# Kernel optimization log

Measured on AMD Instinct MI355X. Metric: run time of the kernel, lower is better.

Reference implementation:

```python
import jax, jax.numpy as jnp
import numpy as np

N_NODES = 50000
N_EDGES = 800000
IN_DIM, HID_DIM, OUT_DIM = 128, 128, 256


def _gcn_conv(x, W, b, src, dst, num_nodes):
    # PyG GCNConv: h = D^{-1/2} (A + I) D^{-1/2} X W + b (self-loops already in src/dst)
    h = x @ W  # (N, F_out)
    ones = jnp.ones(src.shape[0], dtype=h.dtype)
    deg = jax.ops.segment_sum(ones, dst, num_segments=num_nodes)
    dinv = jnp.where(deg > 0, jax.lax.rsqrt(deg), 0.0)
    norm = dinv[src] * dinv[dst]  # (E,)
    msg = h[src] * norm[:, None]  # (E, F_out) gather
    out = jax.ops.segment_sum(msg, dst, num_segments=num_nodes)  # scatter-add
    return out + b


def setup_inputs() -> dict:
    key = jax.random.key(0)
    ks = jax.random.split(key, 6)
    x = jax.random.normal(ks[0], (N_NODES, IN_DIM), dtype=jnp.float32)
    edge_index = jax.random.randint(ks[1], (2, N_EDGES), 0, N_NODES, dtype=jnp.int64)
    W1 = jax.random.normal(ks[2], (IN_DIM, HID_DIM), dtype=jnp.float32) / np.sqrt(IN_DIM)
    b1 = jnp.zeros((HID_DIM,), jnp.float32)
    W2 = jax.random.normal(ks[3], (HID_DIM, OUT_DIM), dtype=jnp.float32) / np.sqrt(HID_DIM)
    b2 = jnp.zeros((OUT_DIM,), jnp.float32)
    Wa = jax.random.normal(ks[4], (OUT_DIM, 1), dtype=jnp.float32) / np.sqrt(OUT_DIM)
    ba = jnp.zeros((1,), jnp.float32)
    return {"x": x, "edge_index": edge_index, "W1": W1, "b1": b1, "W2": W2, "b2": b2, "Wa": Wa, "ba": ba}


def reference(x, edge_index, W1, b1, W2, b2, Wa, ba):
    n = x.shape[0]
    loops = jnp.arange(n, dtype=edge_index.dtype)
    src = jnp.concatenate([edge_index[0], loops])
    dst = jnp.concatenate([edge_index[1], loops])
    h = jax.nn.relu(_gcn_conv(x, W1, b1, src, dst, n))
    # dropout is a no-op in eval mode
    node_embeddings = jax.nn.relu(_gcn_conv(h, W2, b2, src, dst, n))
    logits = node_embeddings @ Wa + ba  # (N, 1)
    attn = jax.nn.softmax(logits, axis=0)  # softmax over nodes
    graph_embedding = jnp.sum(node_embeddings * attn, axis=0, keepdims=True)  # (1, OUT_DIM)
    return (node_embeddings, graph_embedding)
```

## Files before the change

kernel.cpp:

```cpp
#include <hip/hip_runtime.h>
#include <hip/hip_fp16.h>
#include <math.h>

typedef __attribute__((ext_vector_type(8))) short bf16x8;
typedef __attribute__((ext_vector_type(4))) float f32x4;

static __device__ __forceinline__ unsigned short f2bf(float x) {
    unsigned u = __float_as_uint(x);
    unsigned r = (u + 0x7FFF + ((u >> 16) & 1)) >> 16;
    return (unsigned short)r;
}
static __device__ __forceinline__ float bf2f(unsigned short h) {
    return __uint_as_float(((unsigned)h) << 16);
}
static __device__ __forceinline__ void addh8(float a[8], uint4 v) {
    float2 f;
    f = __half22float2(*(const __half2*)&v.x); a[0] += f.x; a[1] += f.y;
    f = __half22float2(*(const __half2*)&v.y); a[2] += f.x; a[3] += f.y;
    f = __half22float2(*(const __half2*)&v.z); a[4] += f.x; a[5] += f.y;
    f = __half22float2(*(const __half2*)&v.w); a[6] += f.x; a[7] += f.y;
}


__global__ __launch_bounds__(256) void count_deg_kernel(const int* __restrict__ dst, int E,
                                                        int* __restrict__ deg,
                                                        int* __restrict__ epos) {
    int e = blockIdx.x * 256 + threadIdx.x;
    if (e < E) epos[e] = atomicAdd(&deg[dst[e]], 1);
}

__global__ __launch_bounds__(256) void scan_partial_kernel(const int* __restrict__ deg, int n,
                                                           int* __restrict__ partials) {
    int idx = blockIdx.x * 1024 + threadIdx.x * 4;
    int4 v = make_int4(0, 0, 0, 0);
    if (idx + 3 < n) v = *(const int4*)(deg + idx);
    else {
        if (idx < n) v.x = deg[idx];
        if (idx + 1 < n) v.y = deg[idx + 1];
        if (idx + 2 < n) v.z = deg[idx + 2];
    }
    int s = v.x + v.y + v.z + v.w;
    for (int off = 1; off < 64; off <<= 1) s += __shfl_xor(s, off);
    __shared__ int sm[4];
    int wave = threadIdx.x >> 6;
    if ((threadIdx.x & 63) == 0) sm[wave] = s;
    __syncthreads();
    if (threadIdx.x == 0) partials[blockIdx.x] = sm[0] + sm[1] + sm[2] + sm[3];
}

__global__ __launch_bounds__(64) void scan_offsets_kernel(const int* __restrict__ partials, int nb,
                                                          int* __restrict__ poff,
                                                          int* __restrict__ rowptr, int n) {
    int t = threadIdx.x;
    int v = (t < nb) ? partials[t] : 0;
    int s = v;
    for (int off = 1; off < 64; off <<= 1) {
        int u = __shfl_up(s, off);
        if (t >= off) s += u;
    }
    poff[t] = s - v;
    if (t == 63) rowptr[n] = s;
}

__global__ __launch_bounds__(256) void scan_final_kernel(const int* __restrict__ deg, int n,
                                                         const int* __restrict__ poff,
                                                         int* __restrict__ rowptr) {
    int idx = blockIdx.x * 1024 + threadIdx.x * 4;
    int4 v = make_int4(0, 0, 0, 0);
    if (idx + 3 < n) v = *(const int4*)(deg + idx);
    else {
        if (idx < n) v.x = deg[idx];
        if (idx + 1 < n) v.y = deg[idx + 1];
        if (idx + 2 < n) v.z = deg[idx + 2];
    }
    int tsum = v.x + v.y + v.z + v.w;
    int lane = threadIdx.x & 63, wave = threadIdx.x >> 6;
    int s = tsum;
    for (int off = 1; off < 64; off <<= 1) {
        int u = __shfl_up(s, off);
        if (lane >= off) s += u;
    }
    __shared__ int wsum[4];
    if (lane == 63) wsum[wave] = s;
    __syncthreads();
    int base = poff[blockIdx.x];
    for (int w = 0; w < wave; ++w) base += wsum[w];
    int e0 = base + s - tsum;
    int4 o;
    o.x = e0; o.y = e0 + v.x; o.z = o.y + v.y; o.w = o.z + v.z;
    if (idx + 3 < n) *(int4*)(rowptr + idx) = o;
    else {
        if (idx < n) rowptr[idx] = o.x;
        if (idx + 1 < n) rowptr[idx + 1] = o.y;
        if (idx + 2 < n) rowptr[idx + 2] = o.z;
    }
}

__global__ __launch_bounds__(256) void scatter_kernel(const int* __restrict__ src,
                                                      const int* __restrict__ dst,
                                                      const int* __restrict__ epos, int E,
                                                      const int* __restrict__ rowptr,
                                                      int* __restrict__ csrsrc) {
    int e = blockIdx.x * 256 + threadIdx.x;
    if (e < E) csrsrc[rowptr[dst[e]] + epos[e]] = src[e];
}


__global__ __launch_bounds__(256) void dinv_prescale_kernel(const float* __restrict__ x,
                                                            const int* __restrict__ deg,
                                                            float* __restrict__ dinv,
                                                            __half2* __restrict__ xs16, int n) {
    int node = blockIdx.x * 4 + (threadIdx.x >> 6);
    int lane = threadIdx.x & 63;
    if (node >= n) return;
    float di = rsqrtf((float)(deg[node] + 1));
    if (lane == 0) dinv[node] = di;
    float2 v = *(const float2*)(x + (size_t)node * 128 + (lane << 1));
    xs16[(size_t)node * 64 + lane] = __floats2half2_rn(di * v.x, di * v.y);
}


__global__ __launch_bounds__(256) void wconvert_kernel(const float* __restrict__ W1,
                                                       const float* __restrict__ W2,
                                                       unsigned short* __restrict__ w1h,
                                                       unsigned short* __restrict__ w1l,
                                                       unsigned short* __restrict__ w2h,
                                                       unsigned short* __restrict__ w2l) {
    int i = blockIdx.x * 256 + threadIdx.x;
    if (i < 128 * 128) {
        int nn = i >> 7, k = i & 127;
        float v = W1[k * 128 + nn];
        unsigned short h = f2bf(v);
        w1h[i] = h;
        w1l[i] = f2bf(v - bf2f(h));
    } else if (i < 128 * 128 + 256 * 128) {
        int j = i - 128 * 128;
        int nn = j >> 7, k = j & 127;
        float v = W2[k * 256 + nn];
        unsigned short h = f2bf(v);
        w2h[j] = h;
        w2l[j] = f2bf(v - bf2f(h));
    }
}


__global__ __launch_bounds__(256) void aggregate_kernel(const unsigned short* __restrict__ X16,
                                                        const float* __restrict__ dinv,
                                                        const int* __restrict__ rowptr,
                                                        const int* __restrict__ deg,
                                                        const int* __restrict__ csrsrc,
                                                        unsigned short* __restrict__ outH,
                                                        unsigned short* __restrict__ outL, int n) {
    int node = blockIdx.x * 16 + (threadIdx.x >> 4);
    int sl = threadIdx.x & 15;
    if (node >= n) return;
    const uint4* Xv = (const uint4*)X16;
    float acc[8] = {0.f, 0.f, 0.f, 0.f, 0.f, 0.f, 0.f, 0.f};
    addh8(acc, Xv[(size_t)node * 16 + sl]);
    int e0 = rowptr[node];
    int e1 = e0 + deg[node];
    int e = e0;
    for (; e + 4 <= e1; e += 4) {
        int s0 = csrsrc[e], s1 = csrsrc[e + 1], s2 = csrsrc[e + 2], s3 = csrsrc[e + 3];
        uint4 v0 = Xv[(size_t)s0 * 16 + sl];
        uint4 v1 = Xv[(size_t)s1 * 16 + sl];
        uint4 v2 = Xv[(size_t)s2 * 16 + sl];
        uint4 v3 = Xv[(size_t)s3 * 16 + sl];
        addh8(acc, v0); addh8(acc, v1); addh8(acc, v2); addh8(acc, v3);
    }
    for (; e < e1; ++e) {
        uint4 v = Xv[(size_t)csrsrc[e] * 16 + sl];
        addh8(acc, v);
    }
    float di = dinv[node];
    unsigned short h[8], l[8];
#pragma unroll
    for (int j = 0; j < 8; ++j) {
        float f = di * acc[j];
        h[j] = f2bf(f);
        l[j] = f2bf(f - bf2f(h[j]));
    }
    uint4 hv, lv;
    hv.x = (unsigned)h[0] | ((unsigned)h[1] << 16);
    hv.y = (unsigned)h[2] | ((unsigned)h[3] << 16);
    hv.z = (unsigned)h[4] | ((unsigned)h[5] << 16);
    hv.w = (unsigned)h[6] | ((unsigned)h[7] << 16);
    lv.x = (unsigned)l[0] | ((unsigned)l[1] << 16);
    lv.y = (unsigned)l[2] | ((unsigned)l[3] << 16);
    lv.z = (unsigned)l[4] | ((unsigned)l[5] << 16);
    lv.w = (unsigned)l[6] | ((unsigned)l[7] << 16);
    *(uint4*)(outH + (size_t)node * 128 + sl * 8) = hv;
    *(uint4*)(outL + (size_t)node * 128 + sl * 8) = lv;
}


template <int N, bool SCALE_DINV, bool DO_LOGITS, bool OUT_F16>
__global__ __launch_bounds__(256, 3) void gemm_mfma(const unsigned short* __restrict__ Ah,
                                                    const unsigned short* __restrict__ Al,
                                                    const unsigned short* __restrict__ Bth,
                                                    const unsigned short* __restrict__ Btl,
                                                    const float* __restrict__ bias,
                                                    void* __restrict__ Cout, int M,
                                                    const float* __restrict__ dinv,
                                                    const float* __restrict__ Wa,
                                                    float* __restrict__ logits) {
    const int t = threadIdx.x;
    const int lane = t & 63;
    const int wave = t >> 6;
    const int wrow = wave >> 1;
    const int wcol = wave & 1;
    const int lq = lane >> 4;
    const int lm = lane & 15;
    const int row0 = blockIdx.x * 128;
    const int col0 = blockIdx.y * 128;

    int ar[4];
#pragma unroll
    for (int rt = 0; rt < 4; ++rt) {
        int r = row0 + wrow * 64 + rt * 16 + lm;
        ar[rt] = (r < M) ? r : (M - 1);
    }
    const int cb = col0 + wcol * 64 + lm;

    f32x4 acc[4][4] = {};
    float lacc[4][4] = {};

#pragma unroll
    for (int kq = 0; kq < 4; ++kq) {
        const int ko = kq * 32 + lq * 8;
        bf16x8 a_h[4], a_l[4], b_h[4], b_l[4];
#pragma unroll
        for (int rt = 0; rt < 4; ++rt) {
            const size_t o = (size_t)ar[rt] * 128 + ko;
            a_h[rt] = *(const bf16x8*)(Ah + o);
            a_l[rt] = *(const bf16x8*)(Al + o);
        }
#pragma unroll
        for (int ct = 0; ct < 4; ++ct) {
            const size_t o = (size_t)(cb + ct * 16) * 128 + ko;
            b_h[ct] = *(const bf16x8*)(Bth + o);
            b_l[ct] = *(const bf16x8*)(Btl + o);
        }
#pragma unroll
        for (int rt = 0; rt < 4; ++rt)
#pragma unroll
            for (int ct = 0; ct < 4; ++ct) {
                acc[rt][ct] = __builtin_amdgcn_mfma_f32_16x16x32_bf16(a_h[rt], b_h[ct], acc[rt][ct], 0, 0, 0);
                acc[rt][ct] = __builtin_amdgcn_mfma_f32_16x16x32_bf16(a_l[rt], b_h[ct], acc[rt][ct], 0, 0, 0);
                acc[rt][ct] = __builtin_amdgcn_mfma_f32_16x16x32_bf16(a_h[rt], b_l[ct], acc[rt][ct], 0, 0, 0);
            }
    }

#pragma unroll
    for (int ct = 0; ct < 4; ++ct) {
        int col = col0 + wcol * 64 + ct * 16 + lm;
        float bc = bias[col];
        float wac = DO_LOGITS ? Wa[col] : 0.f;
#pragma unroll
        for (int rt = 0; rt < 4; ++rt) {
            int rowb = row0 + wrow * 64 + rt * 16 + lq * 4;
#pragma unroll
            for (int reg = 0; reg < 4; ++reg) {
                int gr = rowb + reg;
                if (gr < M) {
                    float o = fmaxf(acc[rt][ct][reg] + bc, 0.f);
                    if (SCALE_DINV) o *= dinv[gr];
                    if (OUT_F16) ((__half*)Cout)[(size_t)gr * N + col] = __float2half(o);
                    else ((float*)Cout)[(size_t)gr * N + col] = o;
                    if (DO_LOGITS) lacc[rt][reg] += o * wac;
                }
            }
        }
    }

    if (DO_LOGITS) {
#pragma unroll
        for (int rt = 0; rt < 4; ++rt)
#pragma unroll
            for (int reg = 0; reg < 4; ++reg) {
                float s = lacc[rt][reg];
                s += __shfl_xor(s, 1);
                s += __shfl_xor(s, 2);
                s += __shfl_xor(s, 4);
                s += __shfl_xor(s, 8);
                int gr = row0 + wrow * 64 + rt * 16 + lq * 4 + reg;
                if (lm == 0 && gr < M) atomicAdd(&logits[gr], s);
            }
    }
}


__global__ __launch_bounds__(256) void maxsum_kernel(const float* __restrict__ logits, int n,
                                                     float2* __restrict__ part) {
    float m = -INFINITY, s = 0.f;
    for (int i = blockIdx.x * 256 + threadIdx.x; i < n; i += gridDim.x * 256) {
        float v = logits[i];
        if (v > m) { s = s * expf(m - v) + 1.f; m = v; }
        else s += expf(v - m);
    }
    __shared__ float sm[256], ss[256];
    sm[threadIdx.x] = m; ss[threadIdx.x] = s;
    __syncthreads();
    for (int off = 128; off > 0; off >>= 1) {
        if (threadIdx.x < off) {
            float m1 = sm[threadIdx.x], s1 = ss[threadIdx.x];
            float m2 = sm[threadIdx.x + off], s2 = ss[threadIdx.x + off];
            float M = fmaxf(m1, m2);
            sm[threadIdx.x] = M;
            ss[threadIdx.x] = s1 * expf(m1 - M) + s2 * expf(m2 - M);
        }
        __syncthreads();
    }
    if (threadIdx.x == 0) part[blockIdx.x] = make_float2(sm[0], ss[0]);
}

__global__ __launch_bounds__(64) void merge_kernel(const float2* __restrict__ part,
                                                   float* __restrict__ gms) {
    __shared__ float sm[64], ss[64];
    float2 p = part[threadIdx.x];
    sm[threadIdx.x] = p.x; ss[threadIdx.x] = p.y;
    __syncthreads();
    for (int off = 32; off > 0; off >>= 1) {
        if (threadIdx.x < off) {
            float m1 = sm[threadIdx.x], s1 = ss[threadIdx.x];
            float m2 = sm[threadIdx.x + off], s2 = ss[threadIdx.x + off];
            float M = fmaxf(m1, m2);
            sm[threadIdx.x] = M;
            ss[threadIdx.x] = s1 * expf(m1 - M) + s2 * expf(m2 - M);
        }
        __syncthreads();
    }
    if (threadIdx.x == 0) { gms[0] = sm[0]; gms[1] = ss[0]; }
}

__global__ __launch_bounds__(256) void weighted_sum_kernel(const float* __restrict__ emb,
                                                           const float* __restrict__ logits,
                                                           const float* __restrict__ gms,
                                                           float* __restrict__ gpart, int n) {
    float g = gms[0];
    int wave = threadIdx.x >> 6;
    int lane = threadIdx.x & 63;
    int stride = gridDim.x * 4;
    float4 acc = make_float4(0.f, 0.f, 0.f, 0.f);
#pragma unroll 2
    for (int r = blockIdx.x * 4 + wave; r < n; r += stride) {
        float w = expf(logits[r] - g);
        float4 v = *(const float4*)(emb + (size_t)r * 256 + (lane << 2));
        acc.x += w * v.x; acc.y += w * v.y; acc.z += w * v.z; acc.w += w * v.w;
    }
    __shared__ float4 sm[256];
    sm[threadIdx.x] = acc;
    __syncthreads();
    if (wave == 0) {
        float4 a = sm[lane], b = sm[64 + lane], c = sm[128 + lane], d = sm[192 + lane];
        float4 s;
        s.x = (a.x + b.x) + (c.x + d.x);
        s.y = (a.y + b.y) + (c.y + d.y);
        s.z = (a.z + b.z) + (c.z + d.z);
        s.w = (a.w + b.w) + (c.w + d.w);
        *(float4*)(gpart + (size_t)blockIdx.x * 256 + (lane << 2)) = s;
    }
}

__global__ __launch_bounds__(256) void reduce_gpart_kernel(const float* __restrict__ gpart,
                                                           float* __restrict__ outTail, int nb) {
    int rows = nb / gridDim.x;
    int r0 = blockIdx.x * rows;
    float s = 0.f;
    for (int r = r0; r < r0 + rows; ++r) s += gpart[(size_t)r * 256 + threadIdx.x];
    atomicAdd(&outTail[threadIdx.x], s);
}

__global__ __launch_bounds__(256) void normalize_kernel(float* __restrict__ outTail,
                                                        const float* __restrict__ gms) {
    outTail[threadIdx.x] = outTail[threadIdx.x] / gms[1];
}


extern "C" void kernel_launch(void* const* d_in, const int* in_sizes, int n_in,
                              void* d_out, int out_size, void* d_ws, size_t ws_size,
                              hipStream_t stream) {
    const float* x  = (const float*)d_in[0];
    const int* ei   = (const int*)d_in[1];
    const float* W1 = (const float*)d_in[2];
    const float* b1 = (const float*)d_in[3];
    const float* W2 = (const float*)d_in[4];
    const float* b2 = (const float*)d_in[5];
    const float* Wa = (const float*)d_in[6];
    float* out = (float*)d_out;

    const int n = in_sizes[0] / 128;
    const int E = in_sizes[1] / 2;
    const int* srcA = ei;
    const int* dstA = ei + E;
    const int nb = (n + 1023) / 1024;
    const int WS_BLOCKS = 1024;

    unsigned short* xs16 = (unsigned short*)d_ws;
    unsigned short* aggH = xs16 + (size_t)n * 128;
    unsigned short* aggL = aggH + (size_t)n * 128;
    unsigned short* w1h  = aggL + (size_t)n * 128;
    unsigned short* w1l  = w1h + 128 * 128;
    unsigned short* w2h  = w1l + 128 * 128;
    unsigned short* w2l  = w2h + 256 * 128;
    float* dinv   = (float*)(w2l + 256 * 128);
    float* logits = dinv + n;
    float2* part  = (float2*)(logits + n);
    float* gms    = (float*)(part + 64);
    float* gpart  = gms + 2;
    int* deg      = (int*)(gpart + WS_BLOCKS * 256);
    int* rowptr   = deg + n;
    int* partials = rowptr + n + 1;
    int* poff     = partials + 64;
    int* epos     = poff + 64;
    int* csrsrc   = epos + E;

    hipMemsetAsync(deg, 0, sizeof(int) * (size_t)n, stream);
    hipMemsetAsync(logits, 0, sizeof(float) * (size_t)n, stream);
    hipMemsetAsync(out + (size_t)n * 256, 0, sizeof(float) * 256, stream);

    count_deg_kernel<<<(E + 255) / 256, 256, 0, stream>>>(dstA, E, deg, epos);
    scan_partial_kernel<<<nb, 256, 0, stream>>>(deg, n, partials);
    scan_offsets_kernel<<<1, 64, 0, stream>>>(partials, nb, poff, rowptr, n);
    scan_final_kernel<<<nb, 256, 0, stream>>>(deg, n, poff, rowptr);
    scatter_kernel<<<(E + 255) / 256, 256, 0, stream>>>(srcA, dstA, epos, E, rowptr, csrsrc);
    dinv_prescale_kernel<<<(n + 3) / 4, 256, 0, stream>>>(x, deg, dinv, (__half2*)xs16, n);
    wconvert_kernel<<<(128 * 128 + 256 * 128 + 255) / 256, 256, 0, stream>>>(W1, W2, w1h, w1l, w2h, w2l);

    int aggBlocks = (n + 15) / 16;
    int gemmRows = (n + 127) / 128;

    aggregate_kernel<<<aggBlocks, 256, 0, stream>>>(xs16, dinv, rowptr, deg, csrsrc, aggH, aggL, n);
    gemm_mfma<128, true, false, true><<<dim3(gemmRows, 1), 256, 0, stream>>>(
        aggH, aggL, w1h, w1l, b1, xs16, n, dinv, nullptr, nullptr);
    aggregate_kernel<<<aggBlocks, 256, 0, stream>>>(xs16, dinv, rowptr, deg, csrsrc, aggH, aggL, n);
    gemm_mfma<256, false, true, false><<<dim3(gemmRows, 2), 256, 0, stream>>>(
        aggH, aggL, w2h, w2l, b2, out, n, nullptr, Wa, logits);

    maxsum_kernel<<<64, 256, 0, stream>>>(logits, n, part);
    merge_kernel<<<1, 64, 0, stream>>>(part, gms);
    weighted_sum_kernel<<<WS_BLOCKS, 256, 0, stream>>>(out, logits, gms, gpart, n);
    reduce_gpart_kernel<<<32, 256, 0, stream>>>(gpart, out + (size_t)n * 256, WS_BLOCKS);
    normalize_kernel<<<1, 256, 0, stream>>>(out + (size_t)n * 256, gms);
}
```

Measured before the change: 333.7 us.

## Stage GEMM A/B tiles through XOR-swizzled LDS instead of direct global loads

Rewrites the MFMA GEMM main loop so each block cooperatively loads 128x32 hi/lo bf16 slices of A and B into shared memory with an XOR swizzle, then each wave reads its fragments from LDS. Before, every wave fetched its fragments straight from global memory, so the same rows were loaded redundantly by waves sharing a row or column. The change adds 32KB of LDS per block and two barriers per k-chunk, which may cut occupancy under the 3-blocks-per-SM launch bound and serializes load and compute without double buffering.

```diff
diff --git a/kernel.cpp b/kernel.cpp
--- a/kernel.cpp
+++ b/kernel.cpp
@@ -204,6 +204,9 @@
                                                     const float* __restrict__ dinv,
                                                     const float* __restrict__ Wa,
                                                     float* __restrict__ logits) {
+    __shared__ unsigned short As[128 * 64];
+    __shared__ unsigned short Bs[128 * 64];
+
     const int t = threadIdx.x;
     const int lane = t & 63;
     const int wave = t >> 6;
@@ -214,40 +217,54 @@
     const int row0 = blockIdx.x * 128;
     const int col0 = blockIdx.y * 128;
 
-    int ar[4];
-#pragma unroll
-    for (int rt = 0; rt < 4; ++rt) {
-        int r = row0 + wrow * 64 + rt * 16 + lm;
-        ar[rt] = (r < M) ? r : (M - 1);
-    }
-    const int cb = col0 + wcol * 64 + lm;
+    const int sg_g = t & 7;
+    const int sg_plane = sg_g >> 2;
+    const int sg_ksub = (sg_g & 3) * 8;
 
     f32x4 acc[4][4] = {};
     float lacc[4][4] = {};
 
-#pragma unroll
-    for (int kq = 0; kq < 4; ++kq) {
-        const int ko = kq * 32 + lq * 8;
-        bf16x8 a_h[4], a_l[4], b_h[4], b_l[4];
+    for (int kc = 0; kc < 4; ++kc) {
+        __syncthreads();
+        const int kbase = kc * 32 + sg_ksub;
+#pragma unroll
+        for (int i = 0; i < 4; ++i) {
+            int r = (t >> 3) + i * 32;
+            int gr = row0 + r;
+            uint4 va = make_uint4(0, 0, 0, 0);
+            if (gr < M) {
+                const unsigned short* srcA = sg_plane ? Al : Ah;
+                va = *(const uint4*)(srcA + (size_t)gr * 128 + kbase);
+            }
+            *(uint4*)(As + r * 64 + (sg_g ^ (r & 7)) * 8) = va;
+            const unsigned short* srcB = sg_plane ? Btl : Bth;
+            uint4 vb = *(const uint4*)(srcB + (size_t)(col0 + r) * 128 + kbase);
+            *(uint4*)(Bs + r * 64 + (sg_g ^ (r & 7)) * 8) = vb;
+        }
+        __syncthreads();
+
+        bf16x8 ah[4], al[4], bh[4], bl[4];
 #pragma unroll
         for (int rt = 0; rt < 4; ++rt) {
-            const size_t o = (size_t)ar[rt] * 128 + ko;
-            a_h[rt] = *(const bf16x8*)(Ah + o);
-            a_l[rt] = *(const bf16x8*)(Al + o);
+            int ra = wrow * 64 + rt * 16 + lm;
+            int base = ra * 64;
+            ah[rt] = *(const bf16x8*)(As + base + ((lq) ^ (ra & 7)) * 8);
+            al[rt] = *(const bf16x8*)(As + base + ((4 + lq) ^ (ra & 7)) * 8);
         }
 #pragma unroll
         for (int ct = 0; ct < 4; ++ct) {
-            const size_t o = (size_t)(cb + ct * 16) * 128 + ko;
-            b_h[ct] = *(const bf16x8*)(Bth + o);
-            b_l[ct] = *(const bf16x8*)(Btl + o);
+            int nb = wcol * 64 + ct * 16 + lm;
+            int base = nb * 64;
+            bh[ct] = *(const bf16x8*)(Bs + base + ((lq) ^ (nb & 7)) * 8);
+            bl[ct] = *(const bf16x8*)(Bs + base + ((4 + lq) ^ (nb & 7)) * 8);
         }
 #pragma unroll
         for (int rt = 0; rt < 4; ++rt)
 #pragma unroll
             for (int ct = 0; ct < 4; ++ct) {
-                acc[rt][ct] = __builtin_amdgcn_mfma_f32_16x16x32_bf16(a_h[rt], b_h[ct], acc[rt][ct], 0, 0, 0);
-                acc[rt][ct] = __builtin_amdgcn_mfma_f32_16x16x32_bf16(a_l[rt], b_h[ct], acc[rt][ct], 0, 0, 0);
-                acc[rt][ct] = __builtin_amdgcn_mfma_f32_16x16x32_bf16(a_h[rt], b_l[ct], acc[rt][ct], 0, 0, 0);
+                acc[rt][ct] = __builtin_amdgcn_mfma_f32_16x16x32_bf16(ah[rt], bh[ct], acc[rt][ct], 0, 0, 0);
+                acc[rt][ct] = __builtin_amdgcn_mfma_f32_16x16x32_bf16(al[rt], bh[ct], acc[rt][ct], 0, 0, 0);
+                acc[rt][ct] = __builtin_amdgcn_mfma_f32_16x16x32_bf16(ah[rt], bl[ct], acc[rt][ct], 0, 0, 0);
             }
     }
 
```

New measurement: 316.2 us. 5.3% less time.
